# Kernel tuning notes

Hardware: AMD Instinct MI355X
Metric: run time of the kernel (lower is better)

## Reference

```python
import jax, jax.numpy as jnp
import numpy as np

D_MODEL = 768
HEADS = 12
D_K = D_MODEL // HEADS
NEG = -1e9


def setup_inputs() -> dict:
    key = jax.random.key(0)
    ks = jax.random.split(key, 12)
    B, S = 1, 4096
    q = jax.random.normal(ks[0], (B, S, D_MODEL), dtype=jnp.float32)
    k = jax.random.normal(ks[1], (B, S, D_MODEL), dtype=jnp.float32)
    v = jax.random.normal(ks[2], (B, S, D_MODEL), dtype=jnp.float32)
    mask = jax.random.randint(ks[3], (B, S, S), 0, 2, dtype=jnp.int32)
    sc = 1.0 / np.sqrt(D_MODEL)
    Wq = jax.random.normal(ks[4], (D_MODEL, D_MODEL), dtype=jnp.float32) * sc
    Wk = jax.random.normal(ks[5], (D_MODEL, D_MODEL), dtype=jnp.float32) * sc
    Wv = jax.random.normal(ks[6], (D_MODEL, D_MODEL), dtype=jnp.float32) * sc
    Wo = jax.random.normal(ks[7], (D_MODEL, D_MODEL), dtype=jnp.float32) * sc
    bq = jnp.zeros((D_MODEL,), jnp.float32)
    bk = jnp.zeros((D_MODEL,), jnp.float32)
    bv = jnp.zeros((D_MODEL,), jnp.float32)
    bo = jnp.zeros((D_MODEL,), jnp.float32)
    return {"q": q, "k": k, "v": v, "Wq": Wq, "bq": bq, "Wk": Wk, "bk": bk,
            "Wv": Wv, "bv": bv, "Wo": Wo, "bo": bo, "mask": mask}


def reference(q, k, v, Wq, bq, Wk, bk, Wv, bv, Wo, bo, mask) -> jnp.ndarray:
    B, S, _ = q.shape
    # projections (x @ W^T + b, matching nn.Linear)
    qh = (q @ Wq.T + bq).reshape(B, S, HEADS, D_K).transpose(0, 2, 1, 3)  # [B,h,S,dk]
    kh = (k @ Wk.T + bk).reshape(B, S, HEADS, D_K).transpose(0, 2, 1, 3)
    vh = (v @ Wv.T + bv).reshape(B, S, HEADS, D_K).transpose(0, 2, 1, 3)
    scores = jnp.einsum('bhqd,bhkd->bhqk', qh, kh) / jnp.sqrt(jnp.float32(D_K))
    scores = jnp.where(mask[:, None, :, :] == 0, jnp.float32(NEG), scores)
    attn = jax.nn.softmax(scores, axis=-1)  # dropout disabled (eval mode)
    ctx = jnp.einsum('bhqk,bhkd->bhqd', attn, vh)
    concat = ctx.transpose(0, 2, 1, 3).reshape(B, S, D_MODEL)
    return concat @ Wo.T + bo
```

## Files before the change

### kernel.cpp

```cpp
#include <hip/hip_runtime.h>

#define S_LEN 4096
#define DMODEL 768
#define NHEADS 12
#define DKH 64
#define SC2F 0.18033688011112042f

typedef __attribute__((ext_vector_type(8))) short bf16x8;
typedef __attribute__((ext_vector_type(4))) float f32x4;
typedef __attribute__((ext_vector_type(16))) float f32x16;
typedef __attribute__((ext_vector_type(4))) short s16x4;

#define AS1 __attribute__((address_space(1)))
#define AS3 __attribute__((address_space(3)))

__device__ __forceinline__ short f2bf(float f) {
    union { float f; unsigned u; } x; x.f = f;
    unsigned r = x.u + 0x7fffu + ((x.u >> 16) & 1u);
    return (short)(r >> 16);
}

__device__ __forceinline__ float bf2f(short s) {
    union { unsigned u; float f; } x;
    x.u = ((unsigned)(unsigned short)s) << 16;
    return x.f;
}

__device__ __forceinline__ void gload_lds16(const void* g, void* l) {
    __builtin_amdgcn_global_load_lds((const AS1 void*)g, (AS3 void*)l, 16, 0, 0);
}

__global__ void cvt_bf16_3(const float* __restrict__ a, const float* __restrict__ b,
                           const float* __restrict__ c, short* __restrict__ da,
                           short* __restrict__ db, short* __restrict__ dc, int n8) {
    const float* s = blockIdx.z == 0 ? a : blockIdx.z == 1 ? b : c;
    short* d = blockIdx.z == 0 ? da : blockIdx.z == 1 ? db : dc;
    int stride = gridDim.x * blockDim.x;
    for (int i = blockIdx.x * blockDim.x + threadIdx.x; i < n8; i += stride) {
        float4 x = ((const float4*)s)[2 * i];
        float4 y = ((const float4*)s)[2 * i + 1];
        bf16x8 o;
        o[0] = f2bf(x.x); o[1] = f2bf(x.y); o[2] = f2bf(x.z); o[3] = f2bf(x.w);
        o[4] = f2bf(y.x); o[5] = f2bf(y.y); o[6] = f2bf(y.z); o[7] = f2bf(y.w);
        ((bf16x8*)d)[i] = o;
    }
}

__global__ void cvt_bf16_4(const float* __restrict__ a, const float* __restrict__ b,
                           const float* __restrict__ c, const float* __restrict__ e,
                           short* __restrict__ dst, int n8) {
    const float* s = blockIdx.z == 0 ? a : blockIdx.z == 1 ? b : blockIdx.z == 2 ? c : e;
    short* d = dst + (size_t)blockIdx.z * (size_t)n8 * 8;
    int stride = gridDim.x * blockDim.x;
    for (int i = blockIdx.x * blockDim.x + threadIdx.x; i < n8; i += stride) {
        float4 x = ((const float4*)s)[2 * i];
        float4 y = ((const float4*)s)[2 * i + 1];
        bf16x8 o;
        o[0] = f2bf(x.x); o[1] = f2bf(x.y); o[2] = f2bf(x.z); o[3] = f2bf(x.w);
        o[4] = f2bf(y.x); o[5] = f2bf(y.y); o[6] = f2bf(y.z); o[7] = f2bf(y.w);
        ((bf16x8*)d)[i] = o;
    }
}

__global__ void pack_mask_k(const int* __restrict__ mask, unsigned long long* __restrict__ mpT, int nwords) {
    int lane = threadIdx.x & 63;
    int wid = (blockIdx.x * blockDim.x + threadIdx.x) >> 6;
    int nw = (gridDim.x * blockDim.x) >> 6;
    for (int w = wid; w < nwords; w += nw) {
        int m = mask[(size_t)w * 64 + lane];
        unsigned long long b = __ballot(m != 0);
        if (lane == 0) mpT[(size_t)(w & 63) * S_LEN + (w >> 6)] = b;
    }
}

__global__ __launch_bounds__(256) void qkv_gemm(
    const short* __restrict__ qA, const short* __restrict__ kA, const short* __restrict__ vA,
    const short* __restrict__ Wqb, const short* __restrict__ Wkb, const short* __restrict__ Wvb,
    const float* __restrict__ bq, const float* __restrict__ bk, const float* __restrict__ bv,
    short* __restrict__ Qh, short* __restrict__ Kh, short* __restrict__ Vt)
{
    const int z = blockIdx.z;
    const short* A = z == 0 ? qA : z == 1 ? kA : vA;
    const short* B = z == 0 ? Wqb : z == 1 ? Wkb : Wvb;
    const float* bias = z == 0 ? bq : z == 1 ? bk : bv;

    __shared__ __align__(16) short As[128 * 64];
    __shared__ __align__(16) short Bs[128 * 64];
    const int tid = threadIdx.x;
    const int wv = tid >> 6, l = tid & 63;
    const int wr = wv >> 1, wc = wv & 1;
    const int g = l >> 4, hl = l & 15;
    const int m0 = blockIdx.x * 128, n0 = blockIdx.y * 128;
    const int Kd = DMODEL;

    f32x4 acc[4][4] = {};

    for (int kt = 0; kt < Kd; kt += 64) {
        __syncthreads();
        #pragma unroll
        for (int i = 0; i < 4; ++i) {
            int row = i * 32 + wv * 8 + (l >> 3);
            int csrc = (l & 7) ^ (row & 7);
            gload_lds16(A + (size_t)(m0 + row) * Kd + kt + csrc * 8, As + (i * 32 + wv * 8) * 64);
        }
        #pragma unroll
        for (int i = 0; i < 4; ++i) {
            int row = i * 32 + wv * 8 + (l >> 3);
            int csrc = (l & 7) ^ (row & 7);
            gload_lds16(B + (size_t)(n0 + row) * Kd + kt + csrc * 8, Bs + (i * 32 + wv * 8) * 64);
        }
        __syncthreads();
        #pragma unroll
        for (int s = 0; s < 2; ++s) {
            bf16x8 af[4], bf[4];
            #pragma unroll
            for (int m = 0; m < 4; ++m) {
                int row = wr * 64 + m * 16 + hl;
                int ch = (s * 4 + g) ^ (row & 7);
                af[m] = *(const bf16x8*)(As + row * 64 + ch * 8);
            }
            #pragma unroll
            for (int n = 0; n < 4; ++n) {
                int row = wc * 64 + n * 16 + hl;
                int ch = (s * 4 + g) ^ (row & 7);
                bf[n] = *(const bf16x8*)(Bs + row * 64 + ch * 8);
            }
            #pragma unroll
            for (int m = 0; m < 4; ++m)
                #pragma unroll
                for (int n = 0; n < 4; ++n)
                    acc[m][n] = __builtin_amdgcn_mfma_f32_16x16x32_bf16(af[m], bf[n], acc[m][n], 0, 0, 0);
        }
    }

    const float scale = (z == 0) ? SC2F : 1.0f;
    #pragma unroll
    for (int m = 0; m < 4; ++m) {
        #pragma unroll
        for (int n = 0; n < 4; ++n) {
            int gsb = m0 + wr * 64 + m * 16 + g * 4;
            int go = n0 + wc * 64 + n * 16 + hl;
            float bvv = bias[go];
            int hh = go >> 6, d = go & 63;
            if (z == 2) {
                s16x4 p;
                #pragma unroll
                for (int r = 0; r < 4; ++r) p[r] = f2bf(acc[m][n][r] + bvv);
                int gsb2 = (gsb & ~12) | ((gsb & 4) << 1) | ((gsb & 8) >> 1);
                *(s16x4*)(Vt + (size_t)hh * DKH * S_LEN + (size_t)d * S_LEN + gsb2) = p;
            } else {
                short* O = z ? Kh : Qh;
                #pragma unroll
                for (int r = 0; r < 4; ++r)
                    O[(size_t)hh * S_LEN * DKH + (size_t)(gsb + r) * DKH + d] = f2bf((acc[m][n][r] + bvv) * scale);
            }
        }
    }
}

__global__ __launch_bounds__(256) void gemm_out(
    const short* __restrict__ A, const short* __restrict__ B,
    const float* __restrict__ bias, float* __restrict__ O)
{
    __shared__ __align__(16) short As[128 * 64];
    __shared__ __align__(16) short Bs[128 * 64];
    const int tid = threadIdx.x;
    const int wv = tid >> 6, l = tid & 63;
    const int wr = wv >> 1, wc = wv & 1;
    const int g = l >> 4, hl = l & 15;
    const int m0 = blockIdx.x * 128, n0 = blockIdx.y * 128;
    const int Kd = DMODEL;

    f32x4 acc[4][4] = {};

    for (int kt = 0; kt < Kd; kt += 64) {
        __syncthreads();
        #pragma unroll
        for (int i = 0; i < 4; ++i) {
            int row = i * 32 + wv * 8 + (l >> 3);
            int csrc = (l & 7) ^ (row & 7);
            gload_lds16(A + (size_t)(m0 + row) * Kd + kt + csrc * 8, As + (i * 32 + wv * 8) * 64);
        }
        #pragma unroll
        for (int i = 0; i < 4; ++i) {
            int row = i * 32 + wv * 8 + (l >> 3);
            int csrc = (l & 7) ^ (row & 7);
            gload_lds16(B + (size_t)(n0 + row) * Kd + kt + csrc * 8, Bs + (i * 32 + wv * 8) * 64);
        }
        __syncthreads();
        #pragma unroll
        for (int s = 0; s < 2; ++s) {
            bf16x8 af[4], bf[4];
            #pragma unroll
            for (int m = 0; m < 4; ++m) {
                int row = wr * 64 + m * 16 + hl;
                int ch = (s * 4 + g) ^ (row & 7);
                af[m] = *(const bf16x8*)(As + row * 64 + ch * 8);
            }
            #pragma unroll
            for (int n = 0; n < 4; ++n) {
                int row = wc * 64 + n * 16 + hl;
                int ch = (s * 4 + g) ^ (row & 7);
                bf[n] = *(const bf16x8*)(Bs + row * 64 + ch * 8);
            }
            #pragma unroll
            for (int m = 0; m < 4; ++m)
                #pragma unroll
                for (int n = 0; n < 4; ++n)
                    acc[m][n] = __builtin_amdgcn_mfma_f32_16x16x32_bf16(af[m], bf[n], acc[m][n], 0, 0, 0);
        }
    }

    #pragma unroll
    for (int m = 0; m < 4; ++m) {
        #pragma unroll
        for (int n = 0; n < 4; ++n) {
            int gsb = m0 + wr * 64 + m * 16 + g * 4;
            int go = n0 + wc * 64 + n * 16 + hl;
            float bvv = bias[go];
            #pragma unroll
            for (int r = 0; r < 4; ++r)
                O[(size_t)(gsb + r) * DMODEL + go] = acc[m][n][r] + bvv;
        }
    }
}

__global__ __launch_bounds__(512) void flash_attn6(
    const short* __restrict__ Qh, const short* __restrict__ Kh,
    const short* __restrict__ Vt, const unsigned long long* __restrict__ mpT,
    short* __restrict__ po, float* __restrict__ pd)
{
    __shared__ __align__(16) char pool[35328];

    const int tid = threadIdx.x;
    const int wv = tid >> 6, l = tid & 63;
    const int wq = wv >> 1, sp = wv & 1;
    const int hi = l >> 5, q = l & 31;

    int fid = blockIdx.x;
    int g = (fid & 7) * 96 + (fid >> 3);
    const int h = g >> 6;
    const int sub = g & 63;
    const int half = sub >> 5;
    const int q0 = (sub & 31) * 128;

    const short* Khb = Kh + (size_t)h * S_LEN * DKH;
    const short* Vtb = Vt + (size_t)h * DKH * S_LEN;
    const int qrow = q0 + wq * 32 + q;

    bf16x8 aq[4];
    #pragma unroll
    for (int s = 0; s < 4; ++s)
        aq[s] = *(const bf16x8*)(Qh + (size_t)h * S_LEN * DKH + (size_t)qrow * DKH + s * 16 + hi * 8);

    f32x16 acc[2] = {};
    float dacc[4] = {0.f, 0.f, 0.f, 0.f};

    short* Kl = (short*)(pool + sp * 8192);
    short* Vl = (short*)(pool + 16384 + sp * 8192);

    for (int i = 0; i < 16; ++i) {
        const int kt = half * 32 + i * 2 + sp;
        const int kv0 = kt * 64;
        __syncthreads();
        #pragma unroll
        for (int j = 0; j < 2; ++j) {
            int rp = (wq * 2 + j) * 4 + (l >> 4);
            int x = (l & 15) ^ (rp & 15);
            int row = rp * 2 + (x >> 3);
            int c = x & 7;
            gload_lds16(Khb + (size_t)(kv0 + row) * DKH + c * 8, Kl + (wq * 2 + j) * 512);
            gload_lds16(Vtb + (size_t)row * S_LEN + kv0 + c * 8, Vl + (wq * 2 + j) * 512);
        }
        unsigned long long w = mpT[(size_t)kt * S_LEN + qrow];
        __syncthreads();

        unsigned long long w2 = w >> (hi * 4);
        unsigned mlo = (unsigned)w2, mhi2 = (unsigned)(w2 >> 32);

        #pragma unroll
        for (int t = 0; t < 2; ++t) {
            const unsigned msk = t ? mhi2 : mlo;
            f32x16 st = {};
            __builtin_amdgcn_s_setprio(1);
            #pragma unroll
            for (int s = 0; s < 4; ++s) {
                int rowb = t * 32 + q;
                int rp = rowb >> 1;
                int ch = (((rowb & 1) << 3) + (s * 2 + hi)) ^ (rp & 15);
                bf16x8 kf = *(const bf16x8*)(Kl + rp * 128 + ch * 8);
                st = __builtin_amdgcn_mfma_f32_32x32x16_bf16(kf, aq[s], st, 0, 0, 0);
            }
            __builtin_amdgcn_s_setprio(0);
            float pf[16];
            #pragma unroll
            for (int r = 0; r < 16; ++r) {
                const int cbit = (r & 3) + 8 * (r >> 2);
                float sv = (msk & (1u << cbit)) ? st[r] : -120.0f;
                pf[r] = __builtin_amdgcn_exp2f(sv);
                dacc[r & 3] += pf[r];
            }
            __builtin_amdgcn_s_setprio(1);
            #pragma unroll
            for (int kk = 0; kk < 2; ++kk) {
                const float* pp = pf + kk * 8;
                union { unsigned u[4]; bf16x8 v; } pa;
                asm("v_cvt_pk_bf16_f32 %0, %1, %2" : "=v"(pa.u[0]) : "v"(pp[0]), "v"(pp[1]));
                asm("v_cvt_pk_bf16_f32 %0, %1, %2" : "=v"(pa.u[1]) : "v"(pp[2]), "v"(pp[3]));
                asm("v_cvt_pk_bf16_f32 %0, %1, %2" : "=v"(pa.u[2]) : "v"(pp[4]), "v"(pp[5]));
                asm("v_cvt_pk_bf16_f32 %0, %1, %2" : "=v"(pa.u[3]) : "v"(pp[6]), "v"(pp[7]));
                const int ks = t * 2 + kk;
                #pragma unroll
                for (int dt = 0; dt < 2; ++dt) {
                    int rowb = dt * 32 + q;
                    int rp = rowb >> 1;
                    int ch = (((rowb & 1) << 3) + (ks * 2 + hi)) ^ (rp & 15);
                    bf16x8 vf = *(const bf16x8*)(Vl + rp * 128 + ch * 8);
                    acc[dt] = __builtin_amdgcn_mfma_f32_32x32x16_bf16(pa.v, vf, acc[dt], 0, 0, 0);
                }
            }
            __builtin_amdgcn_s_setprio(0);
        }
    }

    const float dsum = dacc[0] + dacc[1] + dacc[2] + dacc[3];

    __syncthreads();
    float* accb = (float*)pool;
    float* ddb  = (float*)(pool + 32768);
    ddb[wv * 64 + l] = dsum;
    if (sp == 1) {
        #pragma unroll
        for (int dt = 0; dt < 2; ++dt)
            #pragma unroll
            for (int r = 0; r < 16; ++r)
                accb[(((wq * 2 + dt) * 16 + r) << 6) + l] = acc[dt][r];
    }
    __syncthreads();
    if (sp == 0) {
        float dq = ddb[(wq * 2) * 64 + q] + ddb[(wq * 2) * 64 + 32 + q]
                 + ddb[(wq * 2 + 1) * 64 + q] + ddb[(wq * 2 + 1) * 64 + 32 + q];
        if (hi == 0) pd[(size_t)half * (NHEADS * S_LEN) + (size_t)h * S_LEN + q0 + wq * 32 + q] = dq;
        #pragma unroll
        for (int dt = 0; dt < 2; ++dt) {
            #pragma unroll
            for (int r = 0; r < 16; ++r) {
                float o = acc[dt][r] + accb[(((wq * 2 + dt) * 16 + r) << 6) + l];
                int qo = (r & 3) + 8 * (r >> 2) + 4 * hi;
                po[((size_t)(half * NHEADS + h) * S_LEN + q0 + wq * 32 + qo) * DKH + dt * 32 + q] = f2bf(o);
            }
        }
    }
}

__global__ __launch_bounds__(256) void flash_merge(const short* __restrict__ po,
                                                   const float* __restrict__ pd,
                                                   short* __restrict__ ctx)
{
    const int i = blockIdx.x * 256 + threadIdx.x;
    const int hq = i >> 3;
    const int h = hq >> 12, qrow = hq & 4095;
    bf16x8 a = ((const bf16x8*)po)[i];
    bf16x8 b = ((const bf16x8*)po)[i + NHEADS * S_LEN * DKH / 8];
    float inv = 1.0f / (pd[hq] + pd[NHEADS * S_LEN + hq]);
    bf16x8 o;
    #pragma unroll
    for (int e = 0; e < 8; ++e)
        o[e] = f2bf((bf2f(a[e]) + bf2f(b[e])) * inv);
    *(bf16x8*)(ctx + (size_t)qrow * DMODEL + h * DKH + (i & 7) * 8) = o;
}

extern "C" void kernel_launch(void* const* d_in, const int* in_sizes, int n_in,
                              void* d_out, int out_size, void* d_ws, size_t ws_size,
                              hipStream_t stream) {
    (void)in_sizes; (void)n_in; (void)out_size; (void)ws_size;
    const float* q  = (const float*)d_in[0];
    const float* k  = (const float*)d_in[1];
    const float* v  = (const float*)d_in[2];
    const float* Wq = (const float*)d_in[3];
    const float* bq = (const float*)d_in[4];
    const float* Wk = (const float*)d_in[5];
    const float* bk = (const float*)d_in[6];
    const float* Wv = (const float*)d_in[7];
    const float* bv = (const float*)d_in[8];
    const float* Wo = (const float*)d_in[9];
    const float* bo = (const float*)d_in[10];
    const int* mask = (const int*)d_in[11];

    char* ws = (char*)d_ws;
    short* qb  = (short*)(ws + 0);
    short* kb  = (short*)(ws + 6291456);
    short* vb  = (short*)(ws + 12582912);
    short* Wqb = (short*)(ws + 18874368);
    short* Wkb = (short*)(ws + 20054016);
    short* Wvb = (short*)(ws + 21233664);
    short* Wob = (short*)(ws + 22413312);
    short* Qh  = (short*)(ws + 23592960);
    short* Kh  = (short*)(ws + 29884416);
    short* Vt  = (short*)(ws + 36175872);
    unsigned long long* mpT = (unsigned long long*)(ws + 42467328);
    short* ctx = (short*)(ws + 44564480);
    short* po = (short*)(ws + 0);
    float* pd = (float*)(ws + 12582912);

    const int NQKV8 = S_LEN * DMODEL / 8;
    const int NW8 = DMODEL * DMODEL / 8;
    cvt_bf16_3<<<dim3(512, 1, 3), 256, 0, stream>>>(q, k, v, qb, kb, vb, NQKV8);
    cvt_bf16_4<<<dim3(288, 1, 4), 256, 0, stream>>>(Wq, Wk, Wv, Wo, Wqb, NW8);
    pack_mask_k<<<2048, 256, 0, stream>>>(mask, mpT, S_LEN * S_LEN / 64);

    qkv_gemm<<<dim3(S_LEN / 128, DMODEL / 128, 3), 256, 0, stream>>>(
        qb, kb, vb, Wqb, Wkb, Wvb, bq, bk, bv, Qh, Kh, Vt);

    flash_attn6<<<768, 512, 0, stream>>>(Qh, Kh, Vt, mpT, po, pd);
    flash_merge<<<1536, 256, 0, stream>>>(po, pd, ctx);

    gemm_out<<<dim3(S_LEN / 128, DMODEL / 128), 256, 0, stream>>>(ctx, Wob, bo, (float*)d_out);
}
```

Baseline: 163.9 us.

## Fuse flash merge into output GEMM load and merge prep kernels

Measured after the change: 164.3 us. Within noise of the previous version (+0.3%).

```diff
diff --git a/kernel.cpp b/kernel.cpp
--- a/kernel.cpp
+++ b/kernel.cpp
@@ -30,11 +30,38 @@
     __builtin_amdgcn_global_load_lds((const AS1 void*)g, (AS3 void*)l, 16, 0, 0);
 }
 
-__global__ void cvt_bf16_3(const float* __restrict__ a, const float* __restrict__ b,
-                           const float* __restrict__ c, short* __restrict__ da,
-                           short* __restrict__ db, short* __restrict__ dc, int n8) {
-    const float* s = blockIdx.z == 0 ? a : blockIdx.z == 1 ? b : c;
-    short* d = blockIdx.z == 0 ? da : blockIdx.z == 1 ? db : dc;
+__global__ void cvt_all(const float* __restrict__ q, const float* __restrict__ k,
+                        const float* __restrict__ v, const float* __restrict__ Wq,
+                        const float* __restrict__ Wk, const float* __restrict__ Wv,
+                        const float* __restrict__ Wo,
+                        short* __restrict__ qb, short* __restrict__ kb,
+                        short* __restrict__ vb, short* __restrict__ Wb,
+                        const int* __restrict__ mask, unsigned long long* __restrict__ mpT) {
+    const int z = blockIdx.z;
+    if (z >= 7) {
+        int lane = threadIdx.x & 63;
+        int wid = (blockIdx.x * blockDim.x + threadIdx.x) >> 6;
+        int nw = (gridDim.x * blockDim.x) >> 6;
+        int base = (z - 7) * 65536;
+        for (int w = base + wid; w < base + 65536; w += nw) {
+            int m = mask[(size_t)w * 64 + lane];
+            unsigned long long b = __ballot(m != 0);
+            if (lane == 0) mpT[(size_t)(w & 63) * S_LEN + (w >> 6)] = b;
+        }
+        return;
+    }
+    const float* s;
+    short* d;
+    int n8;
+    if (z < 3) {
+        s = z == 0 ? q : z == 1 ? k : v;
+        d = z == 0 ? qb : z == 1 ? kb : vb;
+        n8 = S_LEN * DMODEL / 8;
+    } else {
+        s = z == 3 ? Wq : z == 4 ? Wk : z == 5 ? Wv : Wo;
+        d = Wb + (size_t)(z - 3) * (DMODEL * DMODEL);
+        n8 = DMODEL * DMODEL / 8;
+    }
     int stride = gridDim.x * blockDim.x;
     for (int i = blockIdx.x * blockDim.x + threadIdx.x; i < n8; i += stride) {
         float4 x = ((const float4*)s)[2 * i];
@@ -43,33 +70,6 @@
         o[0] = f2bf(x.x); o[1] = f2bf(x.y); o[2] = f2bf(x.z); o[3] = f2bf(x.w);
         o[4] = f2bf(y.x); o[5] = f2bf(y.y); o[6] = f2bf(y.z); o[7] = f2bf(y.w);
         ((bf16x8*)d)[i] = o;
-    }
-}
-
-__global__ void cvt_bf16_4(const float* __restrict__ a, const float* __restrict__ b,
-                           const float* __restrict__ c, const float* __restrict__ e,
-                           short* __restrict__ dst, int n8) {
-    const float* s = blockIdx.z == 0 ? a : blockIdx.z == 1 ? b : blockIdx.z == 2 ? c : e;
-    short* d = dst + (size_t)blockIdx.z * (size_t)n8 * 8;
-    int stride = gridDim.x * blockDim.x;
-    for (int i = blockIdx.x * blockDim.x + threadIdx.x; i < n8; i += stride) {
-        float4 x = ((const float4*)s)[2 * i];
-        float4 y = ((const float4*)s)[2 * i + 1];
-        bf16x8 o;
-        o[0] = f2bf(x.x); o[1] = f2bf(x.y); o[2] = f2bf(x.z); o[3] = f2bf(x.w);
-        o[4] = f2bf(y.x); o[5] = f2bf(y.y); o[6] = f2bf(y.z); o[7] = f2bf(y.w);
-        ((bf16x8*)d)[i] = o;
-    }
-}
-
-__global__ void pack_mask_k(const int* __restrict__ mask, unsigned long long* __restrict__ mpT, int nwords) {
-    int lane = threadIdx.x & 63;
-    int wid = (blockIdx.x * blockDim.x + threadIdx.x) >> 6;
-    int nw = (gridDim.x * blockDim.x) >> 6;
-    for (int w = wid; w < nwords; w += nw) {
-        int m = mask[(size_t)w * 64 + lane];
-        unsigned long long b = __ballot(m != 0);
-        if (lane == 0) mpT[(size_t)(w & 63) * S_LEN + (w >> 6)] = b;
     }
 }
 
@@ -159,7 +159,8 @@
 }
 
 __global__ __launch_bounds__(256) void gemm_out(
-    const short* __restrict__ A, const short* __restrict__ B,
+    const short* __restrict__ po, const float* __restrict__ pd,
+    const short* __restrict__ B,
     const float* __restrict__ bias, float* __restrict__ O)
 {
     __shared__ __align__(16) short As[128 * 64];
@@ -175,11 +176,20 @@
 
     for (int kt = 0; kt < Kd; kt += 64) {
         __syncthreads();
+        const int h = kt >> 6;
         #pragma unroll
         for (int i = 0; i < 4; ++i) {
             int row = i * 32 + wv * 8 + (l >> 3);
             int csrc = (l & 7) ^ (row & 7);
-            gload_lds16(A + (size_t)(m0 + row) * Kd + kt + csrc * 8, As + (i * 32 + wv * 8) * 64);
+            size_t base = ((size_t)h * S_LEN + m0 + row) * DKH + csrc * 8;
+            bf16x8 a = *(const bf16x8*)(po + base);
+            bf16x8 b = *(const bf16x8*)(po + (size_t)NHEADS * S_LEN * DKH + base);
+            float inv = 1.0f / (pd[h * S_LEN + m0 + row] + pd[NHEADS * S_LEN + h * S_LEN + m0 + row]);
+            bf16x8 o;
+            #pragma unroll
+            for (int e = 0; e < 8; ++e)
+                o[e] = f2bf((bf2f(a[e]) + bf2f(b[e])) * inv);
+            *(bf16x8*)(As + (i * 32 + wv * 8) * 64 + l * 8) = o;
         }
         #pragma unroll
         for (int i = 0; i < 4; ++i) {
@@ -353,23 +363,6 @@
     }
 }
 
-__global__ __launch_bounds__(256) void flash_merge(const short* __restrict__ po,
-                                                   const float* __restrict__ pd,
-                                                   short* __restrict__ ctx)
-{
-    const int i = blockIdx.x * 256 + threadIdx.x;
-    const int hq = i >> 3;
-    const int h = hq >> 12, qrow = hq & 4095;
-    bf16x8 a = ((const bf16x8*)po)[i];
-    bf16x8 b = ((const bf16x8*)po)[i + NHEADS * S_LEN * DKH / 8];
-    float inv = 1.0f / (pd[hq] + pd[NHEADS * S_LEN + hq]);
-    bf16x8 o;
-    #pragma unroll
-    for (int e = 0; e < 8; ++e)
-        o[e] = f2bf((bf2f(a[e]) + bf2f(b[e])) * inv);
-    *(bf16x8*)(ctx + (size_t)qrow * DMODEL + h * DKH + (i & 7) * 8) = o;
-}
-
 extern "C" void kernel_launch(void* const* d_in, const int* in_sizes, int n_in,
                               void* d_out, int out_size, void* d_ws, size_t ws_size,
                               hipStream_t stream) {
@@ -399,21 +392,15 @@
     short* Kh  = (short*)(ws + 29884416);
     short* Vt  = (short*)(ws + 36175872);
     unsigned long long* mpT = (unsigned long long*)(ws + 42467328);
-    short* ctx = (short*)(ws + 44564480);
     short* po = (short*)(ws + 0);
     float* pd = (float*)(ws + 12582912);
 
-    const int NQKV8 = S_LEN * DMODEL / 8;
-    const int NW8 = DMODEL * DMODEL / 8;
-    cvt_bf16_3<<<dim3(512, 1, 3), 256, 0, stream>>>(q, k, v, qb, kb, vb, NQKV8);
-    cvt_bf16_4<<<dim3(288, 1, 4), 256, 0, stream>>>(Wq, Wk, Wv, Wo, Wqb, NW8);
-    pack_mask_k<<<2048, 256, 0, stream>>>(mask, mpT, S_LEN * S_LEN / 64);
+    cvt_all<<<dim3(512, 1, 11), 256, 0, stream>>>(q, k, v, Wq, Wk, Wv, Wo, qb, kb, vb, Wqb, mask, mpT);
 
     qkv_gemm<<<dim3(S_LEN / 128, DMODEL / 128, 3), 256, 0, stream>>>(
         qb, kb, vb, Wqb, Wkb, Wvb, bq, bk, bv, Qh, Kh, Vt);
 
     flash_attn6<<<768, 512, 0, stream>>>(Qh, Kh, Vt, mpT, po, pd);
-    flash_merge<<<1536, 256, 0, stream>>>(po, pd, ctx);
-
-    gemm_out<<<dim3(S_LEN / 128, DMODEL / 128), 256, 0, stream>>>(ctx, Wob, bo, (float*)d_out);
-}
+
+    gemm_out<<<dim3(S_LEN / 128, DMODEL / 128), 256, 0, stream>>>(po, pd, Wob, bo, (float*)d_out);
+}
```
